# Performance work log

Measured on AMD Instinct MI355X. Metric: run time of the kernel, lower is better.

## Reference

```python
import jax, jax.numpy as jnp
import numpy as np

KS = 3  # kernel_size
PAD = 1
STRIDE = 1
N = KS * KS


def conv2d(x, w, b=None, stride=1, padding=0):
    out = jax.lax.conv_general_dilated(
        x, w, (stride, stride), [(padding, padding), (padding, padding)],
        dimension_numbers=("NCHW", "OIHW", "NCHW"))
    if b is not None:
        out = out + b[None, :, None, None]
    return out


def deform_conv2d(x, pw, pb, w):
    """Deformable conv v1 (no modulation), kernel 3, pad 1, stride 1."""
    B, C, H, W = x.shape
    offset = conv2d(x, pw, pb, stride=STRIDE, padding=1)  # (B, 2N, h, w)
    h, ww = offset.shape[2], offset.shape[3]
    x_pad = jnp.pad(x, ((0, 0), (0, 0), (PAD, PAD), (PAD, PAD)))
    Hp, Wp = x_pad.shape[2], x_pad.shape[3]

    # p = p_0 + p_n + offset  (first N entries are x/rows, last N are y/cols)
    rng = jnp.arange(-(KS - 1) // 2, (KS - 1) // 2 + 1, dtype=x.dtype)
    pn_x, pn_y = jnp.meshgrid(rng, rng, indexing="ij")
    pn = jnp.concatenate([pn_x.reshape(-1), pn_y.reshape(-1)])  # (2N,)
    p0_x = jnp.arange(1, h * STRIDE + 1, STRIDE, dtype=x.dtype)  # (h,)
    p0_y = jnp.arange(1, ww * STRIDE + 1, STRIDE, dtype=x.dtype)  # (w,)
    p0 = jnp.concatenate([
        jnp.broadcast_to(p0_x[None, :, None], (N, h, ww)),
        jnp.broadcast_to(p0_y[None, None, :], (N, h, ww)),
    ], axis=0)  # (2N, h, w)
    p = offset + pn[None, :, None, None] + p0[None]
    p = p.transpose(0, 2, 3, 1)  # (B, h, w, 2N)
    px, py = p[..., :N], p[..., N:]

    fx, fy = jnp.floor(px), jnp.floor(py)
    q_lt_x = jnp.clip(fx, 0, Hp - 1).astype(jnp.int32)
    q_lt_y = jnp.clip(fy, 0, Wp - 1).astype(jnp.int32)
    q_rb_x = jnp.clip(fx + 1, 0, Hp - 1).astype(jnp.int32)
    q_rb_y = jnp.clip(fy + 1, 0, Wp - 1).astype(jnp.int32)

    pxc = jnp.clip(px, 0, Hp - 1)
    pyc = jnp.clip(py, 0, Wp - 1)

    g_lt = (1 + (q_lt_x - pxc)) * (1 + (q_lt_y - pyc))
    g_rb = (1 - (q_rb_x - pxc)) * (1 - (q_rb_y - pyc))
    g_lb = (1 + (q_lt_x - pxc)) * (1 - (q_rb_y - pyc))
    g_rt = (1 - (q_rb_x - pxc)) * (1 + (q_lt_y - pyc))

    gather = jax.vmap(lambda xi, ix, iy: xi[:, ix, iy])  # -> (B, C, h, w, N)
    x_lt = gather(x_pad, q_lt_x, q_lt_y)
    x_rb = gather(x_pad, q_rb_x, q_rb_y)
    x_lb = gather(x_pad, q_lt_x, q_rb_y)
    x_rt = gather(x_pad, q_rb_x, q_lt_y)

    x_off = (g_lt[:, None] * x_lt + g_rb[:, None] * x_rb
             + g_lb[:, None] * x_lb + g_rt[:, None] * x_rt)  # (B,C,h,w,N)

    # (B,C,h,w,ks,ks) -> (B,C,h*ks,w*ks), row offset fills rows, col offset fills cols
    x_off = x_off.reshape(B, C, h, ww, KS, KS).transpose(0, 1, 2, 4, 3, 5)
    x_off = x_off.reshape(B, C, h * KS, ww * KS)
    return conv2d(x_off, w, None, stride=KS, padding=0)


def setup_inputs() -> dict:
    key = jax.random.key(0)
    ks = jax.random.split(key, 9)
    C = 256
    x = jax.random.normal(ks[0], (4, C, 64, 64), dtype=jnp.float32)
    # small offset-conv weights so sampled offsets stay in a realistic range
    pw_x = jax.random.normal(ks[1], (18, C, 3, 3), dtype=jnp.float32) * 0.05
    pb_x = jnp.zeros((18,), jnp.float32)
    w_x = jax.random.normal(ks[2], (C, C, 3, 3), dtype=jnp.float32) * 0.02
    pw_y = jax.random.normal(ks[3], (18, C, 3, 3), dtype=jnp.float32) * 0.05
    pb_y = jnp.zeros((18,), jnp.float32)
    w_y = jax.random.normal(ks[4], (C, C, 3, 3), dtype=jnp.float32) * 0.02
    w_o = jax.random.normal(ks[5], (C, 2 * C, 1, 1), dtype=jnp.float32) * 0.04
    b_o = jnp.zeros((C,), jnp.float32)
    return {"x": x, "pw_x": pw_x, "pb_x": pb_x, "w_x": w_x,
            "pw_y": pw_y, "pb_y": pb_y, "w_y": w_y, "w_o": w_o, "b_o": b_o}


def reference(x, pw_x, pb_x, w_x, pw_y, pb_y, w_y, w_o, b_o):
    conv_x = deform_conv2d(x, pw_x, pb_x, w_x)
    conv_y = deform_conv2d(x, pw_y, pb_y, w_y)
    xy = jnp.concatenate([conv_x, conv_y], axis=1)  # (B, 2C, H, W)
    return conv2d(xy, w_o, b_o) + x
```

## Files before the change

kernel.cpp:

```cpp
#include <hip/hip_runtime.h>

typedef unsigned short u16;
typedef __attribute__((ext_vector_type(8))) short bf16x8;
typedef __attribute__((ext_vector_type(4))) float f32x4;
typedef __attribute__((ext_vector_type(4))) u16 u16x4;

__device__ __forceinline__ unsigned f2bf(float f) {
    unsigned u = __float_as_uint(f);
    return (u + 0x7FFFu + ((u >> 16) & 1u)) >> 16;
}

__device__ __forceinline__ void gll16(const void* g, void* l) {
    __builtin_amdgcn_global_load_lds(
        (const __attribute__((address_space(1))) char*)g,
        (__attribute__((address_space(3))) char*)l, 16, 0, 0);
}

__global__ void k_transpose_w(const float* __restrict__ wx,
                              const float* __restrict__ wy,
                              u16* __restrict__ Apan) {
    int idx = blockIdx.x * 256 + threadIdx.x;
    int br = idx / 589824, rem = idx % 589824;
    int kt = rem / 8192, r2 = rem % 8192;
    int co = r2 / 32, kw = r2 % 32;
    int k = kt * 32 + kw, n9 = k >> 8, ci = k & 255;
    const float* w = br ? wy : wx;
    Apan[idx] = (u16)f2bf(w[(co * 256 + ci) * 9 + n9]);
}

__global__ void k_transpose_wo(const float* __restrict__ wo, u16* __restrict__ Af) {
    int idx = blockIdx.x * 256 + threadIdx.x;
    int kt = idx / 8192, r2 = idx % 8192;
    int co = r2 / 32, kw = r2 % 32;
    Af[idx] = (u16)f2bf(wo[co * 512 + kt * 32 + kw]);
}

__global__ void k_transpose_pw(const float* __restrict__ pwx,
                               const float* __restrict__ pwy,
                               float* __restrict__ pwT) {
    int idx  = blockIdx.x * 256 + threadIdx.x;
    int ch36 = idx % 36;
    int t    = idx / 36;
    int n    = t % 9, ci = t / 9;
    int br   = ch36 / 18, ch = ch36 % 18;
    const float* pw = br ? pwy : pwx;
    pwT[idx] = pw[(ch * 256 + ci) * 9 + n];
}

__global__ __launch_bounds__(256) void k_transpose_x(const float* __restrict__ x,
                                                     float* __restrict__ xT) {
    __shared__ float lds[256 * 65];
    int h = blockIdx.x, b = blockIdx.y;
    int t = threadIdx.x;
    int ci0 = t >> 6, w0 = t & 63;
#pragma unroll 4
    for (int it = 0; it < 64; ++it) {
        int ci = it * 4 + ci0;
        lds[ci * 65 + w0] = x[((b * 256 + ci) * 64 + h) * 64 + w0];
    }
    __syncthreads();
    float* dstrow = xT + (size_t)b * 1115136 + ((h + 1) * 66 + 1) * 256;
#pragma unroll 4
    for (int it = 0; it < 64; ++it)
        dstrow[it * 256 + t] = lds[t * 65 + it];
}

__global__ __launch_bounds__(256) void k_offset_sk(const float* __restrict__ x,
                                                   const float* __restrict__ pwT,
                                                   float* __restrict__ part) {
    __shared__ float rows[396];
    int t = threadIdx.x;
    int h0 = blockIdx.x * 4;
    int b = blockIdx.y, ks = blockIdx.z;
    int r0 = t >> 6, w = t & 63;

    float acc[36];
#pragma unroll
    for (int c = 0; c < 36; ++c) acc[c] = 0.f;

    int ci0 = ks * 32;
    for (int cc = 0; cc < 32; ++cc) {
        int ci = ci0 + cc;
        const float* xc = x + ((b * 256 + ci) * 64) * 64;
        __syncthreads();
        {
            int r = t / 66, c = t % 66;
            int gr = h0 - 1 + r, gc = c - 1;
            float v = 0.f;
            if ((unsigned)gr < 64u && (unsigned)gc < 64u) v = xc[gr * 64 + gc];
            rows[t] = v;
            int t2 = t + 256;
            if (t2 < 396) {
                r = t2 / 66; c = t2 % 66;
                gr = h0 - 1 + r; gc = c - 1;
                v = 0.f;
                if ((unsigned)gr < 64u && (unsigned)gc < 64u) v = xc[gr * 64 + gc];
                rows[t2] = v;
            }
        }
        __syncthreads();
        const float* pw = pwT + ci * 324;
#pragma unroll
        for (int k9 = 0; k9 < 9; ++k9) {
            int ki = k9 / 3, kj = k9 % 3;
            float xv = rows[(r0 + ki) * 66 + w + kj];
#pragma unroll
            for (int c = 0; c < 36; ++c)
                acc[c] += pw[k9 * 36 + c] * xv;
        }
    }
    int pix = (h0 + r0) * 64 + w;
#pragma unroll
    for (int c = 0; c < 36; ++c)
        part[((ks * 4 + b) * 36 + c) * 4096 + pix] = acc[c];
}

__global__ void k_offset_red(const float* __restrict__ part,
                             const float* __restrict__ pbx,
                             const float* __restrict__ pby,
                             float* __restrict__ off) {
    int i = blockIdx.x * 256 + threadIdx.x;
    int pix = i & 4095;
    int ch = (i >> 12) % 18;
    int bb = (i >> 12) / 18;
    int br = bb >> 2, b = bb & 3;
    int ch36 = br * 18 + ch;
    float s = br ? pby[ch] : pbx[ch];
#pragma unroll
    for (int ks = 0; ks < 8; ++ks)
        s += part[((ks * 4 + b) * 36 + ch36) * 4096 + pix];
    off[i] = s;
}

__global__ __launch_bounds__(256) void k_sample_t(const float* __restrict__ xT,
                                                  const float* __restrict__ off,
                                                  u16* __restrict__ Bpan,
                                                  int br, int bp) {
    int t = threadIdx.x;
    int h = blockIdx.x * 4 + (t >> 6);
    int w = t & 63;
    int bloc = blockIdx.y;
    int b = bp * 2 + bloc;
    int z = blockIdx.z;
    int n9 = z % 9, quarter = z / 9;
    int pix = h * 64 + w;

    float offx = off[((br * 4 + b) * 18 + n9) * 4096 + pix];
    float offy = off[((br * 4 + b) * 18 + n9 + 9) * 4096 + pix];
    int ki = n9 / 3, kj = n9 % 3;
    float px = offx + (float)(ki - 1) + (float)(h + 1);
    float py = offy + (float)(kj - 1) + (float)(w + 1);
    float fx = floorf(px), fy = floorf(py);
    int ltx = min(max((int)fx, 0), 65);
    int lty = min(max((int)fy, 0), 65);
    int rbx = min(max((int)fx + 1, 0), 65);
    int rby = min(max((int)fy + 1, 0), 65);
    float pxc = fminf(fmaxf(px, 0.f), 65.f);
    float pyc = fminf(fmaxf(py, 0.f), 65.f);
    float axl = 1.f + ((float)ltx - pxc);
    float axr = 1.f - ((float)rbx - pxc);
    float ayl = 1.f + ((float)lty - pyc);
    float ayr = 1.f - ((float)rby - pyc);
    float glt = axl * ayl, grb = axr * ayr, glb = axl * ayr, grt = axr * ayl;

    const float* base = xT + (size_t)b * 1115136 + quarter * 64;
    const float4* p00 = (const float4*)(base + (ltx * 66 + lty) * 256);
    const float4* p11 = (const float4*)(base + (rbx * 66 + rby) * 256);
    const float4* p01 = (const float4*)(base + (ltx * 66 + rby) * 256);
    const float4* p10 = (const float4*)(base + (rbx * 66 + lty) * 256);

#pragma unroll
    for (int oct = 0; oct < 8; ++oct) {
        unsigned r[4];
#pragma unroll
        for (int q = 0; q < 2; ++q) {
            int cg = oct * 2 + q;
            float4 a = p00[cg], bb = p11[cg], c = p01[cg], d = p10[cg];
            float f0 = glt * a.x + grb * bb.x + glb * c.x + grt * d.x;
            float f1 = glt * a.y + grb * bb.y + glb * c.y + grt * d.y;
            float f2 = glt * a.z + grb * bb.z + glb * c.z + grt * d.z;
            float f3 = glt * a.w + grb * bb.w + glb * c.w + grt * d.w;
            r[q * 2]     = f2bf(f0) | (f2bf(f1) << 16);
            r[q * 2 + 1] = f2bf(f2) | (f2bf(f3) << 16);
        }
        int ci = quarter * 64 + oct * 8;
        int kt = n9 * 8 + (ci >> 5);
        int kw = ci & 31;
        uint4* dst = (uint4*)(Bpan + (kt * 8192 + bloc * 4096 + pix) * 32 + kw);
        *dst = make_uint4(r[0], r[1], r[2], r[3]);
    }
}

__global__ __launch_bounds__(256) void k_gemm_deform(const u16* __restrict__ Apan,
                                                     const u16* __restrict__ Bpan,
                                                     u16* __restrict__ P,
                                                     int br, int bp) {
    __shared__ __align__(16) char lds[24576];
    int t = threadIdx.x;
    int ntile = blockIdx.x, cot = blockIdx.y;
    int wv = t >> 6, l = t & 63;
    int lr = l & 15, lq = l >> 4;
    int wm = (wv >> 1) * 64, wn = (wv & 1) * 32;

    f32x4 acc[4][2];
#pragma unroll
    for (int i = 0; i < 4; ++i)
#pragma unroll
        for (int j = 0; j < 2; ++j) acc[i][j] = (f32x4){0.f, 0.f, 0.f, 0.f};

    auto stg = [&](int buf, int kt) {
        const char* as = (const char*)(Apan + (br * 72 + kt) * 8192 + cot * 4096);
        const char* bs = (const char*)(Bpan + kt * 262144 + ntile * 2048);
        char* al = lds + buf * 8192;
        char* bl = lds + 16384 + buf * 4096;
        gll16(as + wv * 1024 + l * 16, al + wv * 1024);
        gll16(as + 4096 + wv * 1024 + l * 16, al + 4096 + wv * 1024);
        gll16(bs + wv * 1024 + l * 16, bl + wv * 1024);
    };

    stg(0, 0);
    int cur = 0;
    for (int kt = 0; kt < 72; ++kt) {
        __syncthreads();
        if (kt + 1 < 72) stg(cur ^ 1, kt + 1);
        const u16* Ab = (const u16*)(lds + cur * 8192);
        const u16* Bb = (const u16*)(lds + 16384 + cur * 4096);
        bf16x8 af[4], bfv[2];
#pragma unroll
        for (int mf = 0; mf < 4; ++mf)
            af[mf] = *(const bf16x8*)(Ab + (wm + mf * 16 + lr) * 32 + lq * 8);
#pragma unroll
        for (int nf = 0; nf < 2; ++nf)
            bfv[nf] = *(const bf16x8*)(Bb + (wn + nf * 16 + lr) * 32 + lq * 8);
#pragma unroll
        for (int mf = 0; mf < 4; ++mf)
#pragma unroll
            for (int nf = 0; nf < 2; ++nf)
                acc[mf][nf] = __builtin_amdgcn_mfma_f32_16x16x32_bf16(
                    af[mf], bfv[nf], acc[mf][nf], 0, 0, 0);
        cur ^= 1;
    }

    __syncthreads();
    u16 (*E)[136] = (u16(*)[136])lds;
#pragma unroll
    for (int mf = 0; mf < 4; ++mf)
#pragma unroll
        for (int nf = 0; nf < 2; ++nf) {
            int n = wn + nf * 16 + lr;
            int m0 = wm + mf * 16 + lq * 4;
            u16x4 pk;
#pragma unroll
            for (int r = 0; r < 4; ++r)
                pk[r] = (u16)f2bf(acc[mf][nf][r]);
            *(u16x4*)&E[n][m0] = pk;
        }
    __syncthreads();
    int ktl = t >> 6;
    int nl = t & 63;
    int ktbase = br * 8 + cot * 4;
    const uint4* src = (const uint4*)&E[nl][ktl * 32];
    uint4* dst = (uint4*)(P + ((ktbase + ktl) * 16384 + bp * 8192 + ntile * 64 + nl) * 32);
#pragma unroll
    for (int c = 0; c < 4; ++c) dst[c] = src[c];
}

__global__ __launch_bounds__(256) void k_gemm_final(const u16* __restrict__ Af,
                                                    const u16* __restrict__ P,
                                                    const float* __restrict__ bo,
                                                    const float* __restrict__ x,
                                                    float* __restrict__ out) {
    __shared__ __align__(16) char lds[24576];
    int t = threadIdx.x;
    int ntile = blockIdx.x, cot = blockIdx.y;
    int wv = t >> 6, l = t & 63;
    int lr = l & 15, lq = l >> 4;
    int wm = (wv >> 1) * 64, wn = (wv & 1) * 32;

    f32x4 acc[4][2];
#pragma unroll
    for (int i = 0; i < 4; ++i)
#pragma unroll
        for (int j = 0; j < 2; ++j) acc[i][j] = (f32x4){0.f, 0.f, 0.f, 0.f};

    auto stg = [&](int buf, int kt) {
        const char* as = (const char*)(Af + kt * 8192 + cot * 4096);
        const char* bs = (const char*)(P + kt * 524288 + ntile * 2048);
        char* al = lds + buf * 8192;
        char* bl = lds + 16384 + buf * 4096;
        gll16(as + wv * 1024 + l * 16, al + wv * 1024);
        gll16(as + 4096 + wv * 1024 + l * 16, al + 4096 + wv * 1024);
        gll16(bs + wv * 1024 + l * 16, bl + wv * 1024);
    };

    stg(0, 0);
    int cur = 0;
    for (int kt = 0; kt < 16; ++kt) {
        __syncthreads();
        if (kt + 1 < 16) stg(cur ^ 1, kt + 1);
        const u16* Ab = (const u16*)(lds + cur * 8192);
        const u16* Bb = (const u16*)(lds + 16384 + cur * 4096);
        bf16x8 af[4], bfv[2];
#pragma unroll
        for (int mf = 0; mf < 4; ++mf)
            af[mf] = *(const bf16x8*)(Ab + (wm + mf * 16 + lr) * 32 + lq * 8);
#pragma unroll
        for (int nf = 0; nf < 2; ++nf)
            bfv[nf] = *(const bf16x8*)(Bb + (wn + nf * 16 + lr) * 32 + lq * 8);
#pragma unroll
        for (int mf = 0; mf < 4; ++mf)
#pragma unroll
            for (int nf = 0; nf < 2; ++nf)
                acc[mf][nf] = __builtin_amdgcn_mfma_f32_16x16x32_bf16(
                    af[mf], bfv[nf], acc[mf][nf], 0, 0, 0);
        cur ^= 1;
    }

#pragma unroll
    for (int mf = 0; mf < 4; ++mf)
#pragma unroll
        for (int nf = 0; nf < 2; ++nf) {
            int co0 = cot * 128 + wm + mf * 16 + lq * 4;
            int n = ntile * 64 + wn + nf * 16 + lr;
            int b = n >> 12, pix = n & 4095;
#pragma unroll
            for (int r = 0; r < 4; ++r) {
                int co = co0 + r;
                int o = (b * 256 + co) * 4096 + pix;
                out[o] = acc[mf][nf][r] + bo[co] + x[o];
            }
        }
}

extern "C" void kernel_launch(void* const* d_in, const int* in_sizes, int n_in,
                              void* d_out, int out_size, void* d_ws, size_t ws_size,
                              hipStream_t stream) {
    const float* x   = (const float*)d_in[0];
    const float* pwx = (const float*)d_in[1];
    const float* pbx = (const float*)d_in[2];
    const float* wx  = (const float*)d_in[3];
    const float* pwy = (const float*)d_in[4];
    const float* pby = (const float*)d_in[5];
    const float* wy  = (const float*)d_in[6];
    const float* wo  = (const float*)d_in[7];
    const float* bo  = (const float*)d_in[8];
    float* out = (float*)d_out;

    char* ws = (char*)d_ws;
    float* off  = (float*)(ws + 0);
    float* pwT  = (float*)(ws + 2359296);
    u16*   Apan = (u16*)  (ws + 2691072);
    u16*   Af   = (u16*)  (ws + 5050368);
    u16*   P    = (u16*)  (ws + 5312512);
    u16*   Bpan = (u16*)  (ws + 22089728);
    float* part = (float*)(ws + 22089728);
    float* xT   = (float*)(ws + 59838464);

    k_transpose_pw<<<324,  256, 0, stream>>>(pwx, pwy, pwT);
    k_transpose_w <<<4608, 256, 0, stream>>>(wx, wy, Apan);
    k_transpose_wo<<<512,  256, 0, stream>>>(wo, Af);

    hipMemsetAsync(xT, 0, 17842176, stream);
    k_transpose_x <<<dim3(64, 4),    256, 0, stream>>>(x, xT);

    k_offset_sk   <<<dim3(16, 4, 8), 256, 0, stream>>>(x, pwT, part);
    k_offset_red  <<<2304, 256, 0, stream>>>(part, pbx, pby, off);

    for (int br = 0; br < 2; ++br)
        for (int bp = 0; bp < 2; ++bp) {
            k_sample_t    <<<dim3(16, 2, 36), 256, 0, stream>>>(xT, off, Bpan, br, bp);
            k_gemm_deform <<<dim3(128, 2),    256, 0, stream>>>(Apan, Bpan, P, br, bp);
        }

    k_gemm_final  <<<dim3(256, 2),   256, 0, stream>>>(Af, P, bo, x, out);
}
```

Before: 582.8 us.

## Compute offset convolution as bf16 MFMA implicit GEMM over padded NHWC input

Replaces the scalar FP32 split-K offset convolution and its reduction kernel with an implicit-GEMM kernel that uses bf16 MFMA instructions. The transpose kernel now also writes a bf16 padded channels-last copy of x, and the offset weights are packed into a 64-row bf16 panel (36 of them used) for double-buffered global-to-LDS loads. This removes the partial-sum buffer and the separate reduction pass. In exchange it adds an extra memset and bf16 write, and computes the offsets in bf16, which shifts the sampling positions slightly.

```diff
diff --git a/kernel.cpp b/kernel.cpp
--- a/kernel.cpp
+++ b/kernel.cpp
@@ -35,20 +35,22 @@
     Af[idx] = (u16)f2bf(wo[co * 512 + kt * 32 + kw]);
 }
 
-__global__ void k_transpose_pw(const float* __restrict__ pwx,
-                               const float* __restrict__ pwy,
-                               float* __restrict__ pwT) {
-    int idx  = blockIdx.x * 256 + threadIdx.x;
-    int ch36 = idx % 36;
-    int t    = idx / 36;
-    int n    = t % 9, ci = t / 9;
-    int br   = ch36 / 18, ch = ch36 % 18;
-    const float* pw = br ? pwy : pwx;
-    pwT[idx] = pw[(ch * 256 + ci) * 9 + n];
+__global__ void k_transpose_aoff(const float* __restrict__ pwx,
+                                 const float* __restrict__ pwy,
+                                 u16* __restrict__ Aoff) {
+    int idx = blockIdx.x * 256 + threadIdx.x;
+    int kt = idx / 2048, r2 = idx % 2048;
+    int m = r2 / 32, kw = r2 % 32;
+    int k = kt * 32 + kw, n9 = k >> 8, ci = k & 255;
+    float v = 0.f;
+    if (m < 18)      v = pwx[(m * 256 + ci) * 9 + n9];
+    else if (m < 36) v = pwy[((m - 18) * 256 + ci) * 9 + n9];
+    Aoff[idx] = (u16)f2bf(v);
 }
 
 __global__ __launch_bounds__(256) void k_transpose_x(const float* __restrict__ x,
-                                                     float* __restrict__ xT) {
+                                                     float* __restrict__ xT,
+                                                     u16* __restrict__ xTb) {
     __shared__ float lds[256 * 65];
     int h = blockIdx.x, b = blockIdx.y;
     int t = threadIdx.x;
@@ -59,77 +61,83 @@
         lds[ci * 65 + w0] = x[((b * 256 + ci) * 64 + h) * 64 + w0];
     }
     __syncthreads();
-    float* dstrow = xT + (size_t)b * 1115136 + ((h + 1) * 66 + 1) * 256;
+    float* dstrow = xT  + (size_t)b * 1115136 + ((h + 1) * 66 + 1) * 256;
+    u16*   dstb   = xTb + (size_t)b * 1115136 + ((h + 1) * 66 + 1) * 256;
 #pragma unroll 4
-    for (int it = 0; it < 64; ++it)
-        dstrow[it * 256 + t] = lds[t * 65 + it];
-}
-
-__global__ __launch_bounds__(256) void k_offset_sk(const float* __restrict__ x,
-                                                   const float* __restrict__ pwT,
-                                                   float* __restrict__ part) {
-    __shared__ float rows[396];
-    int t = threadIdx.x;
-    int h0 = blockIdx.x * 4;
-    int b = blockIdx.y, ks = blockIdx.z;
-    int r0 = t >> 6, w = t & 63;
-
-    float acc[36];
-#pragma unroll
-    for (int c = 0; c < 36; ++c) acc[c] = 0.f;
-
-    int ci0 = ks * 32;
-    for (int cc = 0; cc < 32; ++cc) {
-        int ci = ci0 + cc;
-        const float* xc = x + ((b * 256 + ci) * 64) * 64;
+    for (int it = 0; it < 64; ++it) {
+        float v = lds[t * 65 + it];
+        dstrow[it * 256 + t] = v;
+        dstb[it * 256 + t]   = (u16)f2bf(v);
+    }
+}
+
+__global__ __launch_bounds__(256) void k_offset_gemm(const u16* __restrict__ Aoff,
+                                                     const u16* __restrict__ xTb,
+                                                     const float* __restrict__ pbx,
+                                                     const float* __restrict__ pby,
+                                                     float* __restrict__ off) {
+    __shared__ __align__(16) char lds[16384];
+    int t = threadIdx.x;
+    int h = blockIdx.x, b = blockIdx.y;
+    int wv = t >> 6, l = t & 63;
+    int lr = l & 15, lq = l >> 4;
+    int wm = (wv >> 1) * 32, wn = (wv & 1) * 32;
+    const u16* xb = xTb + (size_t)b * 1115136;
+    int w = t >> 2, kwq = t & 3;
+
+    f32x4 acc[2][2];
+#pragma unroll
+    for (int i = 0; i < 2; ++i)
+#pragma unroll
+        for (int j = 0; j < 2; ++j) acc[i][j] = (f32x4){0.f, 0.f, 0.f, 0.f};
+
+    auto stg = [&](int buf, int kt) {
+        int n9 = kt >> 3, ci0 = (kt & 7) * 32;
+        int ki = n9 / 3, kj = n9 % 3;
+        gll16(Aoff + kt * 2048 + t * 8, lds + buf * 4096 + wv * 1024);
+        const u16* bs = xb + ((h + ki) * 66 + (w + kj)) * 256 + ci0 + kwq * 8;
+        gll16(bs, lds + 8192 + buf * 4096 + wv * 1024);
+    };
+
+    stg(0, 0);
+    int cur = 0;
+    for (int kt = 0; kt < 72; ++kt) {
         __syncthreads();
-        {
-            int r = t / 66, c = t % 66;
-            int gr = h0 - 1 + r, gc = c - 1;
-            float v = 0.f;
-            if ((unsigned)gr < 64u && (unsigned)gc < 64u) v = xc[gr * 64 + gc];
-            rows[t] = v;
-            int t2 = t + 256;
-            if (t2 < 396) {
-                r = t2 / 66; c = t2 % 66;
-                gr = h0 - 1 + r; gc = c - 1;
-                v = 0.f;
-                if ((unsigned)gr < 64u && (unsigned)gc < 64u) v = xc[gr * 64 + gc];
-                rows[t2] = v;
+        if (kt + 1 < 72) stg(cur ^ 1, kt + 1);
+        const u16* Ab = (const u16*)(lds + cur * 4096);
+        const u16* Bb = (const u16*)(lds + 8192 + cur * 4096);
+        bf16x8 af[2], bfv[2];
+#pragma unroll
+        for (int mf = 0; mf < 2; ++mf)
+            af[mf] = *(const bf16x8*)(Ab + (wm + mf * 16 + lr) * 32 + lq * 8);
+#pragma unroll
+        for (int nf = 0; nf < 2; ++nf)
+            bfv[nf] = *(const bf16x8*)(Bb + (wn + nf * 16 + lr) * 32 + lq * 8);
+#pragma unroll
+        for (int mf = 0; mf < 2; ++mf)
+#pragma unroll
+            for (int nf = 0; nf < 2; ++nf)
+                acc[mf][nf] = __builtin_amdgcn_mfma_f32_16x16x32_bf16(
+                    af[mf], bfv[nf], acc[mf][nf], 0, 0, 0);
+        cur ^= 1;
+    }
+
+#pragma unroll
+    for (int mf = 0; mf < 2; ++mf)
+#pragma unroll
+        for (int nf = 0; nf < 2; ++nf) {
+            int m0 = wm + mf * 16 + lq * 4;
+            int pix = h * 64 + wn + nf * 16 + lr;
+#pragma unroll
+            for (int r = 0; r < 4; ++r) {
+                int m = m0 + r;
+                if (m < 36) {
+                    int br = m / 18, ch = m % 18;
+                    float bias = br ? pby[ch] : pbx[ch];
+                    off[((br * 4 + b) * 18 + ch) * 4096 + pix] = acc[mf][nf][r] + bias;
+                }
             }
         }
-        __syncthreads();
-        const float* pw = pwT + ci * 324;
-#pragma unroll
-        for (int k9 = 0; k9 < 9; ++k9) {
-            int ki = k9 / 3, kj = k9 % 3;
-            float xv = rows[(r0 + ki) * 66 + w + kj];
-#pragma unroll
-            for (int c = 0; c < 36; ++c)
-                acc[c] += pw[k9 * 36 + c] * xv;
-        }
-    }
-    int pix = (h0 + r0) * 64 + w;
-#pragma unroll
-    for (int c = 0; c < 36; ++c)
-        part[((ks * 4 + b) * 36 + c) * 4096 + pix] = acc[c];
-}
-
-__global__ void k_offset_red(const float* __restrict__ part,
-                             const float* __restrict__ pbx,
-                             const float* __restrict__ pby,
-                             float* __restrict__ off) {
-    int i = blockIdx.x * 256 + threadIdx.x;
-    int pix = i & 4095;
-    int ch = (i >> 12) % 18;
-    int bb = (i >> 12) / 18;
-    int br = bb >> 2, b = bb & 3;
-    int ch36 = br * 18 + ch;
-    float s = br ? pby[ch] : pbx[ch];
-#pragma unroll
-    for (int ks = 0; ks < 8; ++ks)
-        s += part[((ks * 4 + b) * 36 + ch36) * 4096 + pix];
-    off[i] = s;
 }
 
 __global__ __launch_bounds__(256) void k_sample_t(const float* __restrict__ xT,
@@ -348,23 +356,23 @@
 
     char* ws = (char*)d_ws;
     float* off  = (float*)(ws + 0);
-    float* pwT  = (float*)(ws + 2359296);
-    u16*   Apan = (u16*)  (ws + 2691072);
-    u16*   Af   = (u16*)  (ws + 5050368);
-    u16*   P    = (u16*)  (ws + 5312512);
-    u16*   Bpan = (u16*)  (ws + 22089728);
-    float* part = (float*)(ws + 22089728);
-    float* xT   = (float*)(ws + 59838464);
-
-    k_transpose_pw<<<324,  256, 0, stream>>>(pwx, pwy, pwT);
-    k_transpose_w <<<4608, 256, 0, stream>>>(wx, wy, Apan);
-    k_transpose_wo<<<512,  256, 0, stream>>>(wo, Af);
-
-    hipMemsetAsync(xT, 0, 17842176, stream);
-    k_transpose_x <<<dim3(64, 4),    256, 0, stream>>>(x, xT);
-
-    k_offset_sk   <<<dim3(16, 4, 8), 256, 0, stream>>>(x, pwT, part);
-    k_offset_red  <<<2304, 256, 0, stream>>>(part, pbx, pby, off);
+    u16*   Apan = (u16*)  (ws + 2359296);
+    u16*   Af   = (u16*)  (ws + 4718592);
+    u16*   Aoff = (u16*)  (ws + 4980736);
+    u16*   P    = (u16*)  (ws + 5275648);
+    u16*   Bpan = (u16*)  (ws + 22052864);
+    float* xT   = (float*)(ws + 59801600);
+    u16*   xTb  = (u16*)  (ws + 77643776);
+
+    k_transpose_w   <<<4608, 256, 0, stream>>>(wx, wy, Apan);
+    k_transpose_wo  <<<512,  256, 0, stream>>>(wo, Af);
+    k_transpose_aoff<<<576,  256, 0, stream>>>(pwx, pwy, Aoff);
+
+    hipMemsetAsync(xT,  0, 17842176, stream);
+    hipMemsetAsync(xTb, 0,  8921088, stream);
+    k_transpose_x <<<dim3(64, 4),  256, 0, stream>>>(x, xT, xTb);
+
+    k_offset_gemm <<<dim3(64, 4),  256, 0, stream>>>(Aoff, xTb, pbx, pby, off);
 
     for (int br = 0; br < 2; ++br)
         for (int bp = 0; bp < 2; ++bp) {
```

Result: faster. 509.5 us (-12.6%).
